# Kernel optimization log

Hardware: AMD Instinct MI355X
Metric: run time of the kernel (lower is better)

## Reference

```python
import jax, jax.numpy as jnp
import numpy as np

INTEGRAL_RESOLUTION = 0.03  # matches self.integral_resolution

S, H, E, G, F = 4096, 3, 512, 3334, 1  # samples, heads, max events, grid points, formulas


def setup_inputs() -> dict:
    key = jax.random.key(0)
    k1, k2, k3, k4, k5, k6 = jax.random.split(key, 6)
    event_features = jax.random.uniform(k1, (S, H, E, F), dtype=jnp.float32)
    event_mask = jax.random.randint(k2, (S, H, E), 0, 2).astype(bool)
    grid_features = jax.random.uniform(k3, (S, H, G, F), dtype=jnp.float32)
    weights = jax.random.normal(k4, (H, F), dtype=jnp.float32)
    bases = jax.random.normal(k5, (H,), dtype=jnp.float32)
    effects = jnp.ones((H, F), dtype=jnp.float32)  # formula effect is +/-1
    return {
        "event_features": event_features,
        "event_mask": event_mask,
        "grid_features": grid_features,
        "weights": weights,
        "bases": bases,
        "effects": effects,
    }


def reference(event_features, event_mask, grid_features, weights, bases, effects):
    # intensity(t, h) = exp(base_h + sum_f w_{h,f} * feature_f(t) * effect_{h,f})
    w_eff = weights * effects  # [H, F]
    # log-intensity at event times: [S, H, E]
    ev_logit = bases[None, :, None] + jnp.einsum('shef,hf->she', event_features, w_eff)
    # log-intensity on the integral grid: [S, H, G]
    gr_logit = bases[None, :, None] + jnp.einsum('shgf,hf->shg', grid_features, w_eff)
    # sum of log(intensity) over valid events (log(exp(x)) = x)
    log_sum = jnp.sum(jnp.where(event_mask, ev_logit, jnp.zeros((), ev_logit.dtype)))
    # Riemann integral of intensity over [0, T_max]
    integral = jnp.asarray(INTEGRAL_RESOLUTION, gr_logit.dtype) * jnp.sum(jnp.exp(gr_logit))
    return log_sum - integral
```

## Files before the change

### kernel.cpp

```cpp
#include <hip/hip_runtime.h>

constexpr int S = 4096;
constexpr int H = 3;
constexpr int E = 512;
constexpr int G = 3334;
constexpr float RES = 0.03f;

constexpr int NBLK = 2048;
constexpr int NTHR = NBLK * 256;
constexpr int NF4E = S * H * E / 4;
constexpr int NF4G = S * H * G / 4;
constexpr int SLOTS = 20;
constexpr int LAST_VALID = NF4G - (SLOTS - 1) * NTHR;

__device__ __forceinline__ float quad_exp(int fidx, float4 y,
                                          float b0, float b1, float b2,
                                          float w0, float w1, float w2) {
    int j = fidx * 4;
    int q = j / G;
    int r = j - q * G;
    int m = q - (q / 3) * 3;
    int hB = (m == 2) ? 0 : (m + 1);
    float bbA = (m == 0) ? b0 : ((m == 1) ? b1 : b2);
    float wwA = (m == 0) ? w0 : ((m == 1) ? w1 : w2);
    float bbB = (hB == 0) ? b0 : ((hB == 1) ? b1 : b2);
    float wwB = (hB == 0) ? w0 : ((hB == 1) ? w1 : w2);
    int lim = G - r;
    float s;
    s  = __expf(bbA + wwA * y.x);
    s += __expf(((1 >= lim) ? bbB : bbA) + ((1 >= lim) ? wwB : wwA) * y.y);
    s += __expf(((2 >= lim) ? bbB : bbA) + ((2 >= lim) ? wwB : wwA) * y.z);
    s += __expf(((3 >= lim) ? bbB : bbA) + ((3 >= lim) ? wwB : wwA) * y.w);
    return s;
}

__global__ __launch_bounds__(256) void logic_model_kernel(
    const float* __restrict__ ev,
    const int*   __restrict__ mask,
    const float* __restrict__ gr,
    const float* __restrict__ w,
    const float* __restrict__ bases,
    const float* __restrict__ eff,
    float* __restrict__ out)
{
    const float b0 = bases[0], b1 = bases[1], b2 = bases[2];
    const float w0 = w[0] * eff[0], w1 = w[1] * eff[1], w2 = w[2] * eff[2];

    const int tid = blockIdx.x * blockDim.x + threadIdx.x;

    const float4* ev4 = (const float4*)ev;
    const int4*   m4  = (const int4*)mask;
    const float4* gr4 = (const float4*)gr;

    float4 x0 = ev4[tid], x1 = ev4[tid + NTHR], x2 = ev4[tid + 2 * NTHR];
    int4   a0 = m4[tid],  a1 = m4[tid + NTHR],  a2 = m4[tid + 2 * NTHR];

    float4 cur[4];
    #pragma unroll
    for (int u = 0; u < 4; ++u) cur[u] = gr4[tid + u * NTHR];

    float acc_ev = 0.f;
    #pragma unroll
    for (int k = 0; k < 3; ++k) {
        int i = tid + k * NTHR;
        float4 x = (k == 0) ? x0 : ((k == 1) ? x1 : x2);
        int4   m = (k == 0) ? a0 : ((k == 1) ? a1 : a2);
        int row = i >> 7;
        int h = row - (row / 3) * 3;
        float bb = (h == 0) ? b0 : ((h == 1) ? b1 : b2);
        float ww = (h == 0) ? w0 : ((h == 1) ? w1 : w2);
        if (m.x) acc_ev += bb + ww * x.x;
        if (m.y) acc_ev += bb + ww * x.y;
        if (m.z) acc_ev += bb + ww * x.z;
        if (m.w) acc_ev += bb + ww * x.w;
    }

    float acc_gr = 0.f;
    #pragma unroll
    for (int b = 1; b < 5; ++b) {
        float4 nxt[4];
        #pragma unroll
        for (int u = 0; u < 4; ++u) {
            int slot = 4 * b + u;
            int idx = tid + slot * NTHR;
            if (slot == SLOTS - 1) idx = min(idx, NF4G - 1);
            nxt[u] = gr4[idx];
        }
        #pragma unroll
        for (int u = 0; u < 4; ++u)
            acc_gr += quad_exp(tid + (4 * (b - 1) + u) * NTHR, cur[u],
                               b0, b1, b2, w0, w1, w2);
        #pragma unroll
        for (int u = 0; u < 4; ++u) cur[u] = nxt[u];
    }
    #pragma unroll
    for (int u = 0; u < 3; ++u)
        acc_gr += quad_exp(tid + (16 + u) * NTHR, cur[u],
                           b0, b1, b2, w0, w1, w2);
    {
        int idx = min(tid + 19 * NTHR, NF4G - 1);
        float t = quad_exp(idx, cur[3], b0, b1, b2, w0, w1, w2);
        acc_gr += (tid < LAST_VALID) ? t : 0.f;
    }

    float v = acc_ev - RES * acc_gr;

    #pragma unroll
    for (int off = 32; off > 0; off >>= 1)
        v += __shfl_down(v, off, 64);

    __shared__ float sdata[4];
    const int wave = threadIdx.x >> 6;
    const int lane = threadIdx.x & 63;
    if (lane == 0) sdata[wave] = v;
    __syncthreads();
    if (threadIdx.x == 0) {
        float t = sdata[0] + sdata[1] + sdata[2] + sdata[3];
        atomicAdd(out, t);
    }
}

extern "C" void kernel_launch(void* const* d_in, const int* in_sizes, int n_in,
                              void* d_out, int out_size, void* d_ws, size_t ws_size,
                              hipStream_t stream) {
    const float* ev    = (const float*)d_in[0];
    const int*   mask  = (const int*)  d_in[1];
    const float* gr    = (const float*)d_in[2];
    const float* wgt   = (const float*)d_in[3];
    const float* bases = (const float*)d_in[4];
    const float* eff   = (const float*)d_in[5];
    float* out = (float*)d_out;

    hipMemsetAsync(out, 0, sizeof(float), stream);

    logic_model_kernel<<<NBLK, 256, 0, stream>>>(ev, mask, gr, wgt, bases, eff, out);
}
```

Measured before the change: 273.2 us.

## Use block-contiguous tiles, deeper grid prefetch, and exp2 with prescaled constants

Each block now reads its own contiguous chunk of the event and grid arrays instead of a whole-grid strided layout. Grid loads are prefetched three groups ahead in a rotating buffer, and sched_barrier calls pin the load and compute order. The exponential becomes a raw exp2 builtin on bases and weights prescaled by log2(e), which removes a multiply per element. The deeper prefetch raises register pressure, and the scheduling barriers can block useful compiler reordering.

```diff
diff --git a/kernel.cpp b/kernel.cpp
--- a/kernel.cpp
+++ b/kernel.cpp
@@ -5,32 +5,40 @@
 constexpr int E = 512;
 constexpr int G = 3334;
 constexpr float RES = 0.03f;
+constexpr float LOG2E = 1.44269504088896340736f;
 
 constexpr int NBLK = 2048;
-constexpr int NTHR = NBLK * 256;
+constexpr int BT   = 256;
+constexpr int NF4G = S * H * G / 4;
+constexpr int GPB  = NF4G / NBLK;
 constexpr int NF4E = S * H * E / 4;
-constexpr int NF4G = S * H * G / 4;
-constexpr int SLOTS = 20;
-constexpr int LAST_VALID = NF4G - (SLOTS - 1) * NTHR;
+constexpr int EPB  = NF4E / NBLK;
+constexpr int TAIL_T = GPB - 19 * BT;
+
+#if __has_builtin(__builtin_amdgcn_exp2f)
+#define EXP2(x) __builtin_amdgcn_exp2f(x)
+#else
+#define EXP2(x) exp2f(x)
+#endif
 
 __device__ __forceinline__ float quad_exp(int fidx, float4 y,
-                                          float b0, float b1, float b2,
-                                          float w0, float w1, float w2) {
+                                          float c0, float c1, float c2,
+                                          float v0, float v1, float v2) {
     int j = fidx * 4;
     int q = j / G;
     int r = j - q * G;
     int m = q - (q / 3) * 3;
     int hB = (m == 2) ? 0 : (m + 1);
-    float bbA = (m == 0) ? b0 : ((m == 1) ? b1 : b2);
-    float wwA = (m == 0) ? w0 : ((m == 1) ? w1 : w2);
-    float bbB = (hB == 0) ? b0 : ((hB == 1) ? b1 : b2);
-    float wwB = (hB == 0) ? w0 : ((hB == 1) ? w1 : w2);
+    float cA = (m == 0) ? c0 : ((m == 1) ? c1 : c2);
+    float vA = (m == 0) ? v0 : ((m == 1) ? v1 : v2);
+    float cB = (hB == 0) ? c0 : ((hB == 1) ? c1 : c2);
+    float vB = (hB == 0) ? v0 : ((hB == 1) ? v1 : v2);
     int lim = G - r;
     float s;
-    s  = __expf(bbA + wwA * y.x);
-    s += __expf(((1 >= lim) ? bbB : bbA) + ((1 >= lim) ? wwB : wwA) * y.y);
-    s += __expf(((2 >= lim) ? bbB : bbA) + ((2 >= lim) ? wwB : wwA) * y.z);
-    s += __expf(((3 >= lim) ? bbB : bbA) + ((3 >= lim) ? wwB : wwA) * y.w);
+    s  = EXP2(cA + vA * y.x);
+    s += EXP2(((1 >= lim) ? cB : cA) + ((1 >= lim) ? vB : vA) * y.y);
+    s += EXP2(((2 >= lim) ? cB : cA) + ((2 >= lim) ? vB : vA) * y.z);
+    s += EXP2(((3 >= lim) ? cB : cA) + ((3 >= lim) ? vB : vA) * y.w);
     return s;
 }
 
@@ -45,62 +53,73 @@
 {
     const float b0 = bases[0], b1 = bases[1], b2 = bases[2];
     const float w0 = w[0] * eff[0], w1 = w[1] * eff[1], w2 = w[2] * eff[2];
+    const float c0 = b0 * LOG2E, c1 = b1 * LOG2E, c2 = b2 * LOG2E;
+    const float v0 = w0 * LOG2E, v1 = w1 * LOG2E, v2 = w2 * LOG2E;
 
-    const int tid = blockIdx.x * blockDim.x + threadIdx.x;
-
+    const int t = threadIdx.x;
     const float4* ev4 = (const float4*)ev;
     const int4*   m4  = (const int4*)mask;
     const float4* gr4 = (const float4*)gr;
 
-    float4 x0 = ev4[tid], x1 = ev4[tid + NTHR], x2 = ev4[tid + 2 * NTHR];
-    int4   a0 = m4[tid],  a1 = m4[tid + NTHR],  a2 = m4[tid + 2 * NTHR];
+    const int ebase = blockIdx.x * EPB + t;
+    const int gbase = blockIdx.x * GPB;
 
-    float4 cur[4];
+    float4 p1x[3]; int4 p1m[3];
     #pragma unroll
-    for (int u = 0; u < 4; ++u) cur[u] = gr4[tid + u * NTHR];
+    for (int u = 0; u < 3; ++u) {
+        p1x[u] = ev4[ebase + u * BT];
+        p1m[u] = m4[ebase + u * BT];
+    }
+    float4 buf[4][4];
+    #pragma unroll
+    for (int g = 0; g < 3; ++g) {
+        #pragma unroll
+        for (int u = 0; u < 4; ++u) {
+            int slot = 4 * g + u;
+            buf[g][u] = gr4[gbase + t + slot * BT];
+        }
+    }
+    __builtin_amdgcn_sched_barrier(0);
 
     float acc_ev = 0.f;
     #pragma unroll
-    for (int k = 0; k < 3; ++k) {
-        int i = tid + k * NTHR;
-        float4 x = (k == 0) ? x0 : ((k == 1) ? x1 : x2);
-        int4   m = (k == 0) ? a0 : ((k == 1) ? a1 : a2);
-        int row = i >> 7;
+    for (int u = 0; u < 3; ++u) {
+        int row = (ebase + u * BT) >> 7;
         int h = row - (row / 3) * 3;
         float bb = (h == 0) ? b0 : ((h == 1) ? b1 : b2);
         float ww = (h == 0) ? w0 : ((h == 1) ? w1 : w2);
+        float4 x = p1x[u]; int4 m = p1m[u];
         if (m.x) acc_ev += bb + ww * x.x;
         if (m.y) acc_ev += bb + ww * x.y;
         if (m.z) acc_ev += bb + ww * x.z;
         if (m.w) acc_ev += bb + ww * x.w;
     }
+    __builtin_amdgcn_sched_barrier(0);
 
     float acc_gr = 0.f;
     #pragma unroll
-    for (int b = 1; b < 5; ++b) {
-        float4 nxt[4];
+    for (int b = 0; b < 5; ++b) {
+        if (b + 3 < 5) {
+            int g = b + 3;
+            #pragma unroll
+            for (int u = 0; u < 4; ++u) {
+                int slot = 4 * g + u;
+                int pos = t + slot * BT;
+                int idx = gbase + ((slot == 19 && t >= TAIL_T) ? 0 : pos);
+                buf[g & 3][u] = gr4[idx];
+            }
+        }
+        __builtin_amdgcn_sched_barrier(0);
         #pragma unroll
         for (int u = 0; u < 4; ++u) {
             int slot = 4 * b + u;
-            int idx = tid + slot * NTHR;
-            if (slot == SLOTS - 1) idx = min(idx, NF4G - 1);
-            nxt[u] = gr4[idx];
+            int pos = t + slot * BT;
+            bool valid = (slot < 19) || (t < TAIL_T);
+            int fidx = gbase + (valid ? pos : 0);
+            float s = quad_exp(fidx, buf[b & 3][u], c0, c1, c2, v0, v1, v2);
+            acc_gr += valid ? s : 0.f;
         }
-        #pragma unroll
-        for (int u = 0; u < 4; ++u)
-            acc_gr += quad_exp(tid + (4 * (b - 1) + u) * NTHR, cur[u],
-                               b0, b1, b2, w0, w1, w2);
-        #pragma unroll
-        for (int u = 0; u < 4; ++u) cur[u] = nxt[u];
-    }
-    #pragma unroll
-    for (int u = 0; u < 3; ++u)
-        acc_gr += quad_exp(tid + (16 + u) * NTHR, cur[u],
-                           b0, b1, b2, w0, w1, w2);
-    {
-        int idx = min(tid + 19 * NTHR, NF4G - 1);
-        float t = quad_exp(idx, cur[3], b0, b1, b2, w0, w1, w2);
-        acc_gr += (tid < LAST_VALID) ? t : 0.f;
+        __builtin_amdgcn_sched_barrier(0);
     }
 
     float v = acc_ev - RES * acc_gr;
@@ -115,8 +134,8 @@
     if (lane == 0) sdata[wave] = v;
     __syncthreads();
     if (threadIdx.x == 0) {
-        float t = sdata[0] + sdata[1] + sdata[2] + sdata[3];
-        atomicAdd(out, t);
+        float s = sdata[0] + sdata[1] + sdata[2] + sdata[3];
+        atomicAdd(out, s);
     }
 }
 
@@ -133,5 +152,5 @@
 
     hipMemsetAsync(out, 0, sizeof(float), stream);
 
-    logic_model_kernel<<<NBLK, 256, 0, stream>>>(ev, mask, gr, wgt, bases, eff, out);
+    logic_model_kernel<<<NBLK, BT, 0, stream>>>(ev, mask, gr, wgt, bases, eff, out);
 }
```

New measurement: 272.0 us. About the same (-0.4%).
